# Performance work log

Hardware: AMD Instinct MI355X
Metric: run time of the kernel (lower is better)

## Reference

```python
import jax, jax.numpy as jnp
import numpy as np

N_NODES = 50000
N_EDGES = 800000
D_IN = 256
D_HID = 256
D_OUT = 128


def setup_inputs() -> dict:
    key = jax.random.key(0)
    ks = jax.random.split(key, 6)
    z = jax.random.normal(ks[0], (N_NODES, D_IN), dtype=jnp.float32)
    edge_index = jax.random.randint(ks[1], (2, N_EDGES), 0, N_NODES, dtype=jnp.int32)
    W1 = jax.random.normal(ks[2], (D_IN, D_HID), dtype=jnp.float32) / np.sqrt(D_IN).astype(np.float32)
    b1 = jnp.zeros((D_HID,), dtype=jnp.float32)
    W2 = jax.random.normal(ks[3], (D_HID, D_OUT), dtype=jnp.float32) / np.sqrt(D_HID).astype(np.float32)
    b2 = jnp.zeros((D_OUT,), dtype=jnp.float32)
    return {"z": z, "edge_index": edge_index, "W1": W1, "b1": b1, "W2": W2, "b2": b2}


def _gcn_conv(x, W, b, src, dst, n_nodes):
    """GCNConv: x' = D^{-1/2} (A + I) D^{-1/2} (x W) + b (symmetric norm, self-loops)."""
    x = x @ W  # [n, d_out] dense transform first (as in PyG GCNConv)
    loop = jnp.arange(n_nodes, dtype=src.dtype)
    s = jnp.concatenate([src, loop])  # add self-loops
    d = jnp.concatenate([dst, loop])
    deg = jax.ops.segment_sum(jnp.ones(s.shape, dtype=x.dtype), d, num_segments=n_nodes)
    dinv = jnp.where(deg > 0, jax.lax.rsqrt(deg), 0.0)
    norm = dinv[s] * dinv[d]  # per-edge symmetric normalization
    msgs = x[s] * norm[:, None]  # gather + scale
    out = jax.ops.segment_sum(msgs, d, num_segments=n_nodes)  # scatter-add
    return out + b


def reference(z, edge_index, W1, b1, W2, b2):
    src, dst = edge_index[0], edge_index[1]
    n = z.shape[0]
    h = jax.nn.relu(_gcn_conv(z, W1, b1, src, dst, n))
    return _gcn_conv(h, W2, b2, src, dst, n)
```

## Files before the change

### kernel.cpp

```cpp
#include <hip/hip_runtime.h>


#define N_NODES 50000
#define N_EDGES 800000
#define D_IN    256
#define D_HID   256
#define D_OUT   128

typedef unsigned int uint32;
typedef unsigned short u16;

typedef __attribute__((ext_vector_type(8))) short bf16x8;
typedef __attribute__((ext_vector_type(4))) float f32x4;

__device__ __forceinline__ u16 f2bf_rne(float f) {
    union { float f; uint32 u; } c; c.f = f;
    uint32 u = c.u;
    u += 0x7FFFu + ((u >> 16) & 1u);
    return (u16)(u >> 16);
}
__device__ __forceinline__ float bf_lo(uint32 p) {
    union { uint32 u; float f; } c; c.u = p << 16; return c.f;
}
__device__ __forceinline__ float bf_hi(uint32 p) {
    union { uint32 u; float f; } c; c.u = p & 0xFFFF0000u; return c.f;
}


__global__ __launch_bounds__(256) void prep_kernel(const float* __restrict__ z,
                                                   const int* __restrict__ dst,
                                                   const float* __restrict__ W1,
                                                   const float* __restrict__ W2,
                                                   u16* __restrict__ zb,
                                                   u16* __restrict__ w1t,
                                                   u16* __restrict__ w2t,
                                                   int* __restrict__ cnt,
                                                   int* __restrict__ rank) {
    const int g = blockIdx.x * 256 + threadIdx.x;
    const int GT = gridDim.x * 256;

    for (int c = g; c < N_NODES * D_IN / 8; c += GT) {
        int i = c * 8;
        float4 a = *(const float4*)(z + i);
        float4 d = *(const float4*)(z + i + 4);
        uint4 pk;
        pk.x = (uint32)f2bf_rne(a.x) | ((uint32)f2bf_rne(a.y) << 16);
        pk.y = (uint32)f2bf_rne(a.z) | ((uint32)f2bf_rne(a.w) << 16);
        pk.z = (uint32)f2bf_rne(d.x) | ((uint32)f2bf_rne(d.y) << 16);
        pk.w = (uint32)f2bf_rne(d.z) | ((uint32)f2bf_rne(d.w) << 16);
        *(uint4*)(zb + i) = pk;
    }
    for (int idx = g; idx < D_IN * D_HID + D_HID * D_OUT; idx += GT) {
        if (idx < D_IN * D_HID) {
            int nrow = idx >> 8, kcol = idx & 255;
            w1t[idx] = f2bf_rne(W1[kcol * D_HID + nrow]);
        } else {
            int j = idx - D_IN * D_HID;
            int nrow = j >> 8, kcol = j & 255;
            w2t[j] = f2bf_rne(W2[kcol * D_OUT + nrow]);
        }
    }
    for (int i = g; i < N_EDGES; i += GT)
        rank[i] = atomicAdd(&cnt[dst[i]], 1);
}


__global__ __launch_bounds__(1024) void scan_kernel(const int* __restrict__ cnt,
                                                    float* __restrict__ dinv,
                                                    int* __restrict__ row_ptr, int n) {
    __shared__ int wtot[16];
    __shared__ int carry_s;
    const int t = threadIdx.x;
    const int lane = t & 63, w = t >> 6;
    if (t == 0) carry_s = 0;
    __syncthreads();

    const int n4 = n >> 2;
    for (int base = 0; base < n4; base += 1024) {
        int i4 = base + t;
        int4 v = make_int4(0, 0, 0, 0);
        if (i4 < n4) v = ((const int4*)cnt)[i4];
        int s = v.x + v.y + v.z + v.w;
        int x = s;
        #pragma unroll
        for (int off = 1; off < 64; off <<= 1) {
            int u = __shfl_up(x, off, 64);
            if (lane >= off) x += u;
        }
        if (lane == 63) wtot[w] = x;
        __syncthreads();

        int wbase = 0;
        #pragma unroll
        for (int j = 0; j < 16; ++j) if (j < w) wbase += wtot[j];
        int excl = carry_s + wbase + x - s;
        if (i4 < n4) {
            int4 rp;
            rp.x = excl;
            rp.y = rp.x + v.x;
            rp.z = rp.y + v.y;
            rp.w = rp.z + v.z;
            ((int4*)row_ptr)[i4] = rp;
            float4 dv;
            dv.x = rsqrtf((float)(v.x + 1));
            dv.y = rsqrtf((float)(v.y + 1));
            dv.z = rsqrtf((float)(v.z + 1));
            dv.w = rsqrtf((float)(v.w + 1));
            ((float4*)dinv)[i4] = dv;
        }
        __syncthreads();
        if (t == 0) {
            int tot = 0;
            #pragma unroll
            for (int j = 0; j < 16; ++j) tot += wtot[j];
            carry_s += tot;
        }
        __syncthreads();
    }
    if (t == 0) row_ptr[n] = carry_s;
}


__global__ void fill_kernel(const int* __restrict__ src, const int* __restrict__ dst,
                            const int* __restrict__ rank, const int* __restrict__ row_ptr,
                            const float* __restrict__ dinv,
                            int2* __restrict__ edata, int n_edges) {
    int i = blockIdx.x * blockDim.x + threadIdx.x;
    if (i < n_edges) {
        int s = src[i], d = dst[i];
        float w = dinv[s] * dinv[d];
        edata[row_ptr[d] + rank[i]] = make_int2(s, __float_as_int(w));
    }
}


template <int NT>
__global__ __launch_bounds__(256, 4) void gemm_bf16_kernel(const u16* __restrict__ A,
                                                           const u16* __restrict__ BT,
                                                           u16* __restrict__ C, int M) {
    const int K = 256;
    __shared__ short As[128 * 32];
    __shared__ short Bs[128 * 32];

    const int m0 = blockIdx.x * 128;
    const int n0 = blockIdx.y * 128;
    const int t  = threadIdx.x;
    const int w  = t >> 6;
    const int lane = t & 63;
    const int lm = lane & 15;
    const int lq = lane >> 4;
    const int wm = w & 1;
    const int wn = w >> 1;

    f32x4 acc[4][4] = {};

    for (int k0 = 0; k0 < K; k0 += 32) {
        #pragma unroll
        for (int j = 0; j < 2; ++j) {
            int c = w * 128 + j * 64 + lane;
            int row = c >> 2;
            int kc = k0 + (c & 3) * 8;
            int gm = m0 + row; if (gm >= M) gm = M - 1;
            const u16* gpa = A  + (size_t)gm * K + kc;
            const u16* gpb = BT + (size_t)(n0 + row) * K + kc;
            __builtin_amdgcn_global_load_lds(
                (const __attribute__((address_space(1))) void*)gpa,
                (__attribute__((address_space(3))) void*)(As + (w * 128 + j * 64) * 8),
                16, 0, 0);
            __builtin_amdgcn_global_load_lds(
                (const __attribute__((address_space(1))) void*)gpb,
                (__attribute__((address_space(3))) void*)(Bs + (w * 128 + j * 64) * 8),
                16, 0, 0);
        }
        __syncthreads();

        bf16x8 af[4], bf[4];
        #pragma unroll
        for (int mt = 0; mt < 4; ++mt)
            af[mt] = *(const bf16x8*)&As[(wm * 64 + mt * 16 + lm) * 32 + lq * 8];
        #pragma unroll
        for (int nt = 0; nt < 4; ++nt)
            bf[nt] = *(const bf16x8*)&Bs[(wn * 64 + nt * 16 + lm) * 32 + lq * 8];

        #pragma unroll
        for (int mt = 0; mt < 4; ++mt)
            #pragma unroll
            for (int nt = 0; nt < 4; ++nt)
                acc[mt][nt] = __builtin_amdgcn_mfma_f32_16x16x32_bf16(
                    af[mt], bf[nt], acc[mt][nt], 0, 0, 0);

        __syncthreads();
    }

    #pragma unroll
    for (int mt = 0; mt < 4; ++mt) {
        #pragma unroll
        for (int r = 0; r < 4; ++r) {
            int gm = m0 + wm * 64 + mt * 16 + lq * 4 + r;
            if (gm < M) {
                #pragma unroll
                for (int nt = 0; nt < 4; ++nt) {
                    int gn = n0 + wn * 64 + nt * 16 + lm;
                    C[(size_t)gm * NT + gn] = f2bf_rne(acc[mt][nt][r]);
                }
            }
        }
    }
}


__device__ __forceinline__ void upd8(float* a, uint4 p, float w) {
    a[0] = fmaf(bf_lo(p.x), w, a[0]);
    a[1] = fmaf(bf_hi(p.x), w, a[1]);
    a[2] = fmaf(bf_lo(p.y), w, a[2]);
    a[3] = fmaf(bf_hi(p.y), w, a[3]);
    a[4] = fmaf(bf_lo(p.z), w, a[4]);
    a[5] = fmaf(bf_hi(p.z), w, a[5]);
    a[6] = fmaf(bf_lo(p.w), w, a[6]);
    a[7] = fmaf(bf_hi(p.w), w, a[7]);
}

template <int D, bool RELU, bool OUTBF>
__global__ __launch_bounds__(256) void aggregate_kernel(const u16* __restrict__ x,
                                                        const int* __restrict__ row_ptr,
                                                        const int2* __restrict__ edata,
                                                        const float* __restrict__ dinv,
                                                        const float* __restrict__ bias,
                                                        void* __restrict__ outp, int n_nodes) {
    constexpr int LPR = D / 8;
    constexpr int EPW = 64 / LPR;
    constexpr int U   = 8 / EPW;

    int node = (blockIdx.x * blockDim.x + threadIdx.x) >> 6;
    if (node >= n_nodes) return;
    const int lane = threadIdx.x & 63;
    const int grp  = lane / LPR;
    const int l    = lane % LPR;

    float acc[U][8];
    #pragma unroll
    for (int u = 0; u < U; ++u)
        #pragma unroll
        for (int j = 0; j < 8; ++j) acc[u][j] = 0.0f;

    if (grp == 0) {
        float di = dinv[node];
        uint4 p = *(const uint4*)(x + (size_t)node * D + l * 8);
        upd8(acc[0], p, di * di);
    }

    const int e0 = row_ptr[node], e1 = row_ptr[node + 1];
    int e = e0;
    for (; e + U * EPW <= e1; e += U * EPW) {
        int2 q[U];
        #pragma unroll
        for (int u = 0; u < U; ++u)
            q[u] = edata[e + u * EPW + grp];
        #pragma unroll
        for (int u = 0; u < U; ++u) {
            uint4 p = *(const uint4*)(x + (size_t)q[u].x * D + l * 8);
            upd8(acc[u], p, __int_as_float(q[u].y));
        }
    }
    for (; e < e1; e += EPW) {
        int ee = e + grp;
        int2 q = (ee < e1) ? edata[ee] : make_int2(node, 0);
        uint4 p = *(const uint4*)(x + (size_t)q.x * D + l * 8);
        upd8(acc[0], p, __int_as_float(q.y));
    }

    float v[8];
    #pragma unroll
    for (int j = 0; j < 8; ++j) {
        float s = acc[0][j];
        #pragma unroll
        for (int u = 1; u < U; ++u) s += acc[u][j];
        v[j] = s;
    }

    #pragma unroll
    for (int m = LPR; m < 64; m <<= 1)
        #pragma unroll
        for (int j = 0; j < 8; ++j)
            v[j] += __shfl_xor(v[j], m, 64);

    if (grp == 0) {
        #pragma unroll
        for (int j = 0; j < 8; ++j) {
            float s = v[j] + bias[l * 8 + j];
            v[j] = RELU ? fmaxf(s, 0.0f) : s;
        }
        if constexpr (OUTBF) {
            u16* op = (u16*)outp + (size_t)node * D + l * 8;
            uint4 pk;
            pk.x = (uint32)f2bf_rne(v[0]) | ((uint32)f2bf_rne(v[1]) << 16);
            pk.y = (uint32)f2bf_rne(v[2]) | ((uint32)f2bf_rne(v[3]) << 16);
            pk.z = (uint32)f2bf_rne(v[4]) | ((uint32)f2bf_rne(v[5]) << 16);
            pk.w = (uint32)f2bf_rne(v[6]) | ((uint32)f2bf_rne(v[7]) << 16);
            *(uint4*)op = pk;
        } else {
            float* op = (float*)outp + (size_t)node * D + l * 8;
            float4 a = make_float4(v[0], v[1], v[2], v[3]);
            float4 b = make_float4(v[4], v[5], v[6], v[7]);
            *(float4*)op = a;
            *(float4*)(op + 4) = b;
        }
    }
}


extern "C" void kernel_launch(void* const* d_in, const int* in_sizes, int n_in,
                              void* d_out, int out_size, void* d_ws, size_t ws_size,
                              hipStream_t stream) {
    const float* z  = (const float*)d_in[0];
    const int*   ei = (const int*)d_in[1];
    const float* W1 = (const float*)d_in[2];
    const float* b1 = (const float*)d_in[3];
    const float* W2 = (const float*)d_in[4];
    const float* b2 = (const float*)d_in[5];
    float* out = (float*)d_out;

    const int Nn = N_NODES, E = N_EDGES;
    const int* srcp = ei;
    const int* dstp = ei + E;

    char* ws = (char*)d_ws;
    size_t off = 0;
    auto alloc = [&](size_t bytes) -> char* {
        char* p = ws + off;
        off += (bytes + 511) & ~(size_t)511;
        return p;
    };
    u16*   zb     = (u16*)  alloc((size_t)Nn * D_IN * 2);
    u16*   w1t    = (u16*)  alloc((size_t)D_IN * D_HID * 2);
    u16*   w2t    = (u16*)  alloc((size_t)D_HID * D_OUT * 2);
    u16*   x1b    = (u16*)  alloc((size_t)Nn * D_HID * 2);
    u16*   hb     = (u16*)  alloc((size_t)Nn * D_HID * 2);
    u16*   h2b    = (u16*)  alloc((size_t)Nn * D_OUT * 2);
    int*   cnt    = (int*)  alloc((size_t)Nn * 4);
    float* dinv   = (float*)alloc((size_t)Nn * 4);
    int*   row_ptr= (int*)  alloc((size_t)(Nn + 1) * 4);
    int*   rank   = (int*)  alloc((size_t)E * 4);
    int2*  edata  = (int2*) alloc((size_t)E * 8);

    hipMemsetAsync(cnt, 0, (size_t)Nn * 4, stream);
    prep_kernel<<<1024, 256, 0, stream>>>(z, dstp, W1, W2, zb, w1t, w2t, cnt, rank);
    scan_kernel<<<1, 1024, 0, stream>>>(cnt, dinv, row_ptr, Nn);
    fill_kernel<<<(E + 255) / 256, 256, 0, stream>>>(srcp, dstp, rank, row_ptr, dinv, edata, E);
    {
        dim3 grid((Nn + 127) / 128, D_HID / 128);
        gemm_bf16_kernel<D_HID><<<grid, 256, 0, stream>>>(zb, w1t, x1b, Nn);
    }
    {
        int blocks = (Nn + 3) / 4;
        aggregate_kernel<D_HID, true, true><<<blocks, 256, 0, stream>>>(x1b, row_ptr, edata, dinv, b1, hb, Nn);
    }
    {
        dim3 grid((Nn + 127) / 128, D_OUT / 128);
        gemm_bf16_kernel<D_OUT><<<grid, 256, 0, stream>>>(hb, w2t, h2b, Nn);
    }
    {
        int blocks = (Nn + 3) / 4;
        aggregate_kernel<D_OUT, false, false><<<blocks, 256, 0, stream>>>(h2b, row_ptr, edata, dinv, b2, out, Nn);
    }
}
```

Baseline: 301.5 us.

## Store node features in 32-column chunked layout and aggregate per column slice

The GEMMs now write their bf16 outputs in a column-chunked layout: each 32-column slice is stored contiguously across all nodes. The second GEMM reads its input in that layout too. Aggregation becomes a sliced kernel in which each block handles one 32-column chunk for a group of nodes, with 8 lanes per edge and 8-byte gathers. Neighbouring blocks cover different chunks, so each gathered slice is smaller and more likely to stay cache-resident, at the cost of re-reading edge lists once per chunk. Edge data is loaded with non-temporal hints.

```diff
diff --git a/kernel.cpp b/kernel.cpp
--- a/kernel.cpp
+++ b/kernel.cpp
@@ -134,7 +134,7 @@
 }
 
 
-template <int NT>
+template <int NT, bool ACH>
 __global__ __launch_bounds__(256, 4) void gemm_bf16_kernel(const u16* __restrict__ A,
                                                            const u16* __restrict__ BT,
                                                            u16* __restrict__ C, int M) {
@@ -161,7 +161,11 @@
             int row = c >> 2;
             int kc = k0 + (c & 3) * 8;
             int gm = m0 + row; if (gm >= M) gm = M - 1;
-            const u16* gpa = A  + (size_t)gm * K + kc;
+            const u16* gpa;
+            if constexpr (ACH)
+                gpa = A + (size_t)(kc >> 5) * (size_t)M * 32 + (size_t)gm * 32 + (kc & 31);
+            else
+                gpa = A + (size_t)gm * K + kc;
             const u16* gpb = BT + (size_t)(n0 + row) * K + kc;
             __builtin_amdgcn_global_load_lds(
                 (const __attribute__((address_space(1))) void*)gpa,
@@ -201,7 +205,8 @@
                 #pragma unroll
                 for (int nt = 0; nt < 4; ++nt) {
                     int gn = n0 + wn * 64 + nt * 16 + lm;
-                    C[(size_t)gm * NT + gn] = f2bf_rne(acc[mt][nt][r]);
+                    C[(size_t)(gn >> 5) * (size_t)M * 32 + (size_t)gm * 32 + (gn & 31)]
+                        = f2bf_rne(acc[mt][nt][r]);
                 }
             }
         }
@@ -209,101 +214,92 @@
 }
 
 
-__device__ __forceinline__ void upd8(float* a, uint4 p, float w) {
+__device__ __forceinline__ void upd4(float* a, uint2 p, float w) {
     a[0] = fmaf(bf_lo(p.x), w, a[0]);
     a[1] = fmaf(bf_hi(p.x), w, a[1]);
     a[2] = fmaf(bf_lo(p.y), w, a[2]);
     a[3] = fmaf(bf_hi(p.y), w, a[3]);
-    a[4] = fmaf(bf_lo(p.z), w, a[4]);
-    a[5] = fmaf(bf_hi(p.z), w, a[5]);
-    a[6] = fmaf(bf_lo(p.w), w, a[6]);
-    a[7] = fmaf(bf_hi(p.w), w, a[7]);
 }
 
 template <int D, bool RELU, bool OUTBF>
-__global__ __launch_bounds__(256) void aggregate_kernel(const u16* __restrict__ x,
+__global__ __launch_bounds__(256) void aggregate_sliced(const u16* __restrict__ x,
                                                         const int* __restrict__ row_ptr,
-                                                        const int2* __restrict__ edata,
+                                                        const long long* __restrict__ edata,
                                                         const float* __restrict__ dinv,
                                                         const float* __restrict__ bias,
                                                         void* __restrict__ outp, int n_nodes) {
-    constexpr int LPR = D / 8;
-    constexpr int EPW = 64 / LPR;
-    constexpr int U   = 8 / EPW;
-
-    int node = (blockIdx.x * blockDim.x + threadIdx.x) >> 6;
-    if (node >= n_nodes) return;
-    const int lane = threadIdx.x & 63;
-    const int grp  = lane / LPR;
-    const int l    = lane % LPR;
-
-    float acc[U][8];
-    #pragma unroll
-    for (int u = 0; u < U; ++u)
-        #pragma unroll
-        for (int j = 0; j < 8; ++j) acc[u][j] = 0.0f;
-
-    if (grp == 0) {
-        float di = dinv[node];
-        uint4 p = *(const uint4*)(x + (size_t)node * D + l * 8);
-        upd8(acc[0], p, di * di);
-    }
-
-    const int e0 = row_ptr[node], e1 = row_ptr[node + 1];
-    int e = e0;
-    for (; e + U * EPW <= e1; e += U * EPW) {
-        int2 q[U];
-        #pragma unroll
-        for (int u = 0; u < U; ++u)
-            q[u] = edata[e + u * EPW + grp];
-        #pragma unroll
-        for (int u = 0; u < U; ++u) {
-            uint4 p = *(const uint4*)(x + (size_t)q[u].x * D + l * 8);
-            upd8(acc[u], p, __int_as_float(q[u].y));
-        }
-    }
-    for (; e < e1; e += EPW) {
-        int ee = e + grp;
-        int2 q = (ee < e1) ? edata[ee] : make_int2(node, 0);
-        uint4 p = *(const uint4*)(x + (size_t)q.x * D + l * 8);
-        upd8(acc[0], p, __int_as_float(q.y));
-    }
-
-    float v[8];
-    #pragma unroll
-    for (int j = 0; j < 8; ++j) {
-        float s = acc[0][j];
-        #pragma unroll
-        for (int u = 1; u < U; ++u) s += acc[u][j];
-        v[j] = s;
-    }
-
-    #pragma unroll
-    for (int m = LPR; m < 64; m <<= 1)
-        #pragma unroll
-        for (int j = 0; j < 8; ++j)
-            v[j] += __shfl_xor(v[j], m, 64);
-
-    if (grp == 0) {
-        #pragma unroll
-        for (int j = 0; j < 8; ++j) {
-            float s = v[j] + bias[l * 8 + j];
-            v[j] = RELU ? fmaxf(s, 0.0f) : s;
-        }
-        if constexpr (OUTBF) {
-            u16* op = (u16*)outp + (size_t)node * D + l * 8;
-            uint4 pk;
-            pk.x = (uint32)f2bf_rne(v[0]) | ((uint32)f2bf_rne(v[1]) << 16);
-            pk.y = (uint32)f2bf_rne(v[2]) | ((uint32)f2bf_rne(v[3]) << 16);
-            pk.z = (uint32)f2bf_rne(v[4]) | ((uint32)f2bf_rne(v[5]) << 16);
-            pk.w = (uint32)f2bf_rne(v[6]) | ((uint32)f2bf_rne(v[7]) << 16);
-            *(uint4*)op = pk;
-        } else {
-            float* op = (float*)outp + (size_t)node * D + l * 8;
-            float4 a = make_float4(v[0], v[1], v[2], v[3]);
-            float4 b = make_float4(v[4], v[5], v[6], v[7]);
-            *(float4*)op = a;
-            *(float4*)(op + 4) = b;
+    constexpr int NCH = D / 32;
+    constexpr int NSL = 8 / NCH;
+
+    const int slot  = blockIdx.x & 7;
+    const int chunk = slot & (NCH - 1);
+    const int wv    = threadIdx.x >> 6;
+    const int lane  = threadIdx.x & 63;
+    const int grp   = lane >> 3;
+    const int l     = lane & 7;
+    const int nb    = (int)(blockIdx.x >> 3) * (32 * NSL) + (slot / NCH) * 32 + wv * 8;
+
+    const u16* __restrict__ xc = x + (size_t)chunk * (size_t)n_nodes * 32;
+    const float4 bch = *(const float4*)(bias + chunk * 32 + l * 4);
+
+    for (int r = 0; r < 8; ++r) {
+        const int node = nb + r;
+        if (node >= n_nodes) return;
+
+        const float di = dinv[node];
+        const int e0 = row_ptr[node], e1 = row_ptr[node + 1];
+
+        float a0[4], a1[4];
+        {
+            uint2 ps = *(const uint2*)(xc + (size_t)node * 32 + l * 4);
+            float w = (grp == 0) ? di * di : 0.0f;
+            a0[0] = bf_lo(ps.x) * w; a0[1] = bf_hi(ps.x) * w;
+            a0[2] = bf_lo(ps.y) * w; a0[3] = bf_hi(ps.y) * w;
+            a1[0] = 0.0f; a1[1] = 0.0f; a1[2] = 0.0f; a1[3] = 0.0f;
+        }
+
+        int e = e0;
+        for (; e + 16 <= e1; e += 16) {
+            long long q0 = __builtin_nontemporal_load(&edata[e + grp]);
+            long long q1 = __builtin_nontemporal_load(&edata[e + 8 + grp]);
+            uint2 p0 = *(const uint2*)(xc + (size_t)(int)q0 * 32 + l * 4);
+            uint2 p1 = *(const uint2*)(xc + (size_t)(int)q1 * 32 + l * 4);
+            upd4(a0, p0, __int_as_float((int)(q0 >> 32)));
+            upd4(a1, p1, __int_as_float((int)(q1 >> 32)));
+        }
+        for (; e < e1; e += 8) {
+            int ee = e + grp;
+            long long q = 0;
+            if (ee < e1) q = __builtin_nontemporal_load(&edata[ee]);
+            uint2 p = *(const uint2*)(xc + (size_t)(int)q * 32 + l * 4);
+            upd4(a0, p, __int_as_float((int)(q >> 32)));
+        }
+
+        float v[4];
+        #pragma unroll
+        for (int j = 0; j < 4; ++j) v[j] = a0[j] + a1[j];
+        #pragma unroll
+        for (int m = 8; m < 64; m <<= 1)
+            #pragma unroll
+            for (int j = 0; j < 4; ++j) v[j] += __shfl_xor(v[j], m, 64);
+
+        if (grp == 0) {
+            v[0] += bch.x; v[1] += bch.y; v[2] += bch.z; v[3] += bch.w;
+            if (RELU) {
+                #pragma unroll
+                for (int j = 0; j < 4; ++j) v[j] = fmaxf(v[j], 0.0f);
+            }
+            if constexpr (OUTBF) {
+                u16* op = (u16*)outp + (size_t)chunk * (size_t)n_nodes * 32
+                                      + (size_t)node * 32 + l * 4;
+                uint2 pk;
+                pk.x = (uint32)f2bf_rne(v[0]) | ((uint32)f2bf_rne(v[1]) << 16);
+                pk.y = (uint32)f2bf_rne(v[2]) | ((uint32)f2bf_rne(v[3]) << 16);
+                *(uint2*)op = pk;
+            } else {
+                float* op = (float*)outp + (size_t)node * D + chunk * 32 + l * 4;
+                *(float4*)op = make_float4(v[0], v[1], v[2], v[3]);
+            }
         }
     }
 }
@@ -349,18 +345,20 @@
     fill_kernel<<<(E + 255) / 256, 256, 0, stream>>>(srcp, dstp, rank, row_ptr, dinv, edata, E);
     {
         dim3 grid((Nn + 127) / 128, D_HID / 128);
-        gemm_bf16_kernel<D_HID><<<grid, 256, 0, stream>>>(zb, w1t, x1b, Nn);
+        gemm_bf16_kernel<D_HID, false><<<grid, 256, 0, stream>>>(zb, w1t, x1b, Nn);
     }
     {
-        int blocks = (Nn + 3) / 4;
-        aggregate_kernel<D_HID, true, true><<<blocks, 256, 0, stream>>>(x1b, row_ptr, edata, dinv, b1, hb, Nn);
+        int blocks = ((Nn + 31) / 32) * 8;
+        aggregate_sliced<D_HID, true, true><<<blocks, 256, 0, stream>>>(
+            x1b, row_ptr, (const long long*)edata, dinv, b1, hb, Nn);
     }
     {
         dim3 grid((Nn + 127) / 128, D_OUT / 128);
-        gemm_bf16_kernel<D_OUT><<<grid, 256, 0, stream>>>(hb, w2t, h2b, Nn);
+        gemm_bf16_kernel<D_OUT, true><<<grid, 256, 0, stream>>>(hb, w2t, h2b, Nn);
     }
     {
-        int blocks = (Nn + 3) / 4;
-        aggregate_kernel<D_OUT, false, false><<<blocks, 256, 0, stream>>>(h2b, row_ptr, edata, dinv, b2, out, Nn);
-    }
-}
+        int blocks = ((Nn + 63) / 64) * 8;
+        aggregate_sliced<D_OUT, false, false><<<blocks, 256, 0, stream>>>(
+            h2b, row_ptr, (const long long*)edata, dinv, b2, out, Nn);
+    }
+}
```

New measurement: 445.8 us. 47.9% more time.
